# Kernel tuning notes

Hardware: AMD Instinct MI355X
Metric: run time of the kernel (lower is better)

The kernel has to match this reference:

```python
import jax, jax.numpy as jnp
import numpy as np

SOLVER_STEPS = 4  # fixed-step Euler steps per ODE solve (solver_step)


def setup_inputs() -> dict:
    key = jax.random.key(0)
    ks = jax.random.split(key, 10)
    B, T, D, H = 256, 1024, 128, 512
    sd = 1.0 / np.sqrt(H)
    n = lambda k, shape, scale: (jax.random.normal(k, shape, jnp.float32) * scale)
    return {
        "x": n(ks[0], (B, T, D), 1.0),
        "t": jax.random.uniform(ks[1], (B, T, 1), jnp.float32),
        # torch.nn.LSTMCell parameters (gate order: input, forget, cell, output)
        "W_ih": n(ks[2], (4 * H, D), sd),
        "W_hh": n(ks[3], (4 * H, H), sd),
        "b_ih": n(ks[4], (4 * H,), sd),
        "b_hh": n(ks[5], (4 * H,), sd),
        # DiffeqConcat drift MLP: (H+1) -> H -> H, Tanh activation
        "w1": n(ks[6], (H, H + 1), 1.0 / np.sqrt(H + 1)),
        "b1": n(ks[7], (H,), 0.01),
        "w2": n(ks[8], (H, H), sd),
        "b2": n(ks[9], (H,), 0.01),
    }


def _drift(y, s, w1, b1, w2, b2):
    # MLP(concat([s, y])): s is the (scalar) integration time in [0, 1]
    inp = jnp.concatenate([jnp.full_like(y[..., :1], s), y], axis=-1)
    return jnp.tanh(inp @ w1.T + b1) @ w2.T + b2


def _ode_evolve(h, t_i, w1, b1, w2, b2):
    # Integrate dy/ds = t_i * f(s, y) for s in [0, 1] with fixed-step Euler
    # (torchdiffeq time-rescaling trick used by ODEModel/DiffeqConcat).
    dt = 1.0 / SOLVER_STEPS
    y = h
    for k in range(SOLVER_STEPS):
        y = y + dt * t_i * _drift(y, k * dt, w1, b1, w2, b2)  # t_i: (B,1) broadcasts
    return y


def _lstm_cell(x_i, c, h, W_ih, W_hh, b_ih, b_hh):
    gates = x_i @ W_ih.T + b_ih + h @ W_hh.T + b_hh  # (B, 4H)
    i, f, g, o = jnp.split(gates, 4, axis=-1)
    c_new = jax.nn.sigmoid(f) * c + jax.nn.sigmoid(i) * jnp.tanh(g)
    h_new = jax.nn.sigmoid(o) * jnp.tanh(c_new)
    return c_new, h_new


def reference(x, t, W_ih, W_hh, b_ih, b_hh, w1, b1, w2, b2):
    B, T, D = x.shape
    H = W_hh.shape[1]

    def step(carry, inp):
        c, h = carry
        x_i, t_i = inp  # (B, D), (B, 1)
        h_pre = _ode_evolve(h, t_i, w1, b1, w2, b2)
        c, h = _lstm_cell(x_i, c, h, W_ih, W_hh, b_ih, b_hh)
        return (c, h), h_pre

    init = (jnp.zeros((B, H), x.dtype), jnp.zeros((B, H), x.dtype))
    xs = (jnp.swapaxes(x, 0, 1), jnp.swapaxes(t, 0, 1))  # time-major for scan
    _, hiddens = jax.lax.scan(step, init, xs)  # (T, B, H)
    return jnp.swapaxes(hiddens, 0, 1)  # (B, T, H)
```

## Files before the change

kernel.cpp:

```cpp
#include <hip/hip_runtime.h>
#include <stdint.h>

#define B_  256
#define T_  1024
#define D_  128
#define H_  512
#define G4_ 2048
#define BT_ (B_ * T_)

#define NG_ 16
#define NC_ 16

typedef unsigned short u16;
typedef __attribute__((ext_vector_type(8))) short    bf16x8;
typedef __attribute__((ext_vector_type(8))) u16      u16x8;
typedef __attribute__((ext_vector_type(4))) float    f32x4;
typedef __attribute__((ext_vector_type(4))) uint32_t u32x4;

static __device__ __forceinline__ u16 f2bf(float f) {
  uint32_t u = __builtin_bit_cast(uint32_t, f);
  u += 0x7FFFu + ((u >> 16) & 1u);
  return (u16)(u >> 16);
}

static __device__ __forceinline__ u16x8 pack8(float4 a, float4 b) {
  u16x8 p;
  p[0] = f2bf(a.x); p[1] = f2bf(a.y); p[2] = f2bf(a.z); p[3] = f2bf(a.w);
  p[4] = f2bf(b.x); p[5] = f2bf(b.y); p[6] = f2bf(b.z); p[7] = f2bf(b.w);
  return p;
}

static __device__ __forceinline__ float fast_sig(float x) {
  return 1.f / (1.f + __expf(-x));
}
static __device__ __forceinline__ float fast_tanh(float x) {
  return 1.f - 2.f / (__expf(2.f * x) + 1.f);
}

__global__ void prep_kernel(const float* __restrict__ Whh, const float* __restrict__ Wih,
                            const float* __restrict__ w1,  const float* __restrict__ w2,
                            const float* __restrict__ b_ih, const float* __restrict__ b_hh,
                            u16* __restrict__ Whh_bf, u16* __restrict__ Wih_bf,
                            u16* __restrict__ w1y_bf, u16* __restrict__ w2_bf,
                            float* __restrict__ w1s, float* __restrict__ bsum,
                            uint32_t* __restrict__ flags, float* __restrict__ Yd) {
  const int idx = blockIdx.x * blockDim.x + threadIdx.x;
  if (idx < G4_ * H_) Whh_bf[idx] = f2bf(Whh[idx]);
  if (idx < G4_ * D_) Wih_bf[idx] = f2bf(Wih[idx]);
  if (idx < H_ * H_) {
    const int n = idx >> 9, k = idx & 511;
    w1y_bf[idx] = f2bf(w1[n * 513 + 1 + k]);
    w2_bf[idx]  = f2bf(w2[idx]);
  }
  if (idx < H_)  w1s[idx]  = w1[idx * 513];
  if (idx < G4_) bsum[idx] = b_ih[idx] + b_hh[idx];
  if (idx < T_ * NG_ * 4) flags[idx] = 0;
  if (idx < B_ * H_) {
    const int b = idx >> 9, h = idx & 511;
    Yd[(size_t)b * T_ * H_ + h] = 0.f;
  }
}

__launch_bounds__(256)
__global__ void lstm_persist2(const float* __restrict__ x,
                              const u16* __restrict__ Whh_bf,
                              const u16* __restrict__ Wih_bf,
                              const float* __restrict__ bsum,
                              float* __restrict__ Yd,
                              u16* __restrict__ xchh,
                              uint32_t* __restrict__ flags) {
  __shared__ u16   As[16][648];
  __shared__ float Gs[4][16][34];

  const int tid  = threadIdx.x;
  const int lane = tid & 63;
  const int gw   = tid >> 6;
  const int w    = blockIdx.x;
  const int g    = (w & 7) * 2 + (w >> 7);
  const int c    = (w >> 3) & 15;
  const int br0  = g * 16;
  const int hc0  = c * 32;

  const int cl = lane & 15;
  const int ko = (lane >> 4) * 8;

  bf16x8 wf0[20], wf1[20];
  {
    const int j0 = gw * H_ + hc0 + cl;
#pragma unroll
    for (int kt = 0; kt < 16; ++kt) {
      wf0[kt] = *(const bf16x8*)(Whh_bf + (size_t)j0 * H_ + kt * 32 + ko);
      wf1[kt] = *(const bf16x8*)(Whh_bf + (size_t)(j0 + 16) * H_ + kt * 32 + ko);
    }
#pragma unroll
    for (int kt = 0; kt < 4; ++kt) {
      wf0[16 + kt] = *(const bf16x8*)(Wih_bf + (size_t)j0 * D_ + kt * 32 + ko);
      wf1[16 + kt] = *(const bf16x8*)(Wih_bf + (size_t)(j0 + 16) * D_ + kt * 32 + ko);
    }
  }

  const int er = tid >> 4;
  const int ec = (tid & 15) * 2;
  const int jb = hc0 + ec;
  float c0 = 0.f, c1 = 0.f;
  const float bi0 = bsum[jb],            bi1 = bsum[jb + 1];
  const float bf0 = bsum[H_ + jb],       bf1 = bsum[H_ + jb + 1];
  const float bg0 = bsum[2 * H_ + jb],   bg1 = bsum[2 * H_ + jb + 1];
  const float bo0 = bsum[3 * H_ + jb],   bo1 = bsum[3 * H_ + jb + 1];

  const int xr  = tid & 15,  xk  = tid >> 4;
  const int pr  = tid >> 4,  pcb = tid & 15;

  for (int s = 0; s < T_ - 1; ++s) {
    {
      const float4* x4 = (const float4*)(x + ((size_t)(br0 + xr) * T_ + s) * D_ + xk * 8);
      float4 a = x4[0], b = x4[1];
      *(u16x8*)&As[xr][512 + xk * 8] = pack8(a, b);
    }

    if (s == 0) {
      u16x8 z = {};
#pragma unroll
      for (int i = 0; i < 4; ++i) *(u16x8*)&As[pr][pcb * 32 + i * 8] = z;
    } else {
      const char* fp = (const char*)flags + ((size_t)s * NG_ + g) * 16;
      u32x4 f;
      do {
        asm volatile("global_load_dwordx4 %0, %1, off sc0 sc1\n\ts_waitcnt vmcnt(0)"
                     : "=&v"(f) : "v"(fp) : "memory");
      } while (f[0] != 0xA5A5A5A5u || f[1] != 0xA5A5A5A5u ||
               f[2] != 0xA5A5A5A5u || f[3] != 0xA5A5A5A5u);
      const char* hb = (const char*)xchh + (((size_t)(s & 1) * NG_ + g) << 14) + tid * 64;
      u32x4 h0, h1, h2, h3;
      asm volatile(
        "global_load_dwordx4 %0, %4, off sc0 sc1\n\t"
        "global_load_dwordx4 %1, %4, off offset:16 sc0 sc1\n\t"
        "global_load_dwordx4 %2, %4, off offset:32 sc0 sc1\n\t"
        "global_load_dwordx4 %3, %4, off offset:48 sc0 sc1\n\t"
        "s_waitcnt vmcnt(0)"
        : "=&v"(h0), "=&v"(h1), "=&v"(h2), "=&v"(h3)
        : "v"(hb) : "memory");
      *(u16x8*)&As[pr][pcb * 32]      = __builtin_bit_cast(u16x8, h0);
      *(u16x8*)&As[pr][pcb * 32 + 8]  = __builtin_bit_cast(u16x8, h1);
      *(u16x8*)&As[pr][pcb * 32 + 16] = __builtin_bit_cast(u16x8, h2);
      *(u16x8*)&As[pr][pcb * 32 + 24] = __builtin_bit_cast(u16x8, h3);
    }
    __syncthreads();

    f32x4 acc0 = {}, acc1 = {};
#pragma unroll
    for (int kt = 0; kt < 20; ++kt) {
      bf16x8 a = *(const bf16x8*)&As[cl][kt * 32 + ko];
      acc0 = __builtin_amdgcn_mfma_f32_16x16x32_bf16(a, wf0[kt], acc0, 0, 0, 0);
      acc1 = __builtin_amdgcn_mfma_f32_16x16x32_bf16(a, wf1[kt], acc1, 0, 0, 0);
    }

    {
      const int rr = (lane >> 4) * 4;
#pragma unroll
      for (int r = 0; r < 4; ++r) {
        Gs[gw][rr + r][cl]      = acc0[r];
        Gs[gw][rr + r][16 + cl] = acc1[r];
      }
    }
    __syncthreads();

    {
      const float2 gi = *(const float2*)&Gs[0][er][ec];
      const float2 gf = *(const float2*)&Gs[1][er][ec];
      const float2 gg = *(const float2*)&Gs[2][er][ec];
      const float2 go = *(const float2*)&Gs[3][er][ec];
      c0 = fast_sig(gf.x + bf0) * c0 + fast_sig(gi.x + bi0) * fast_tanh(gg.x + bg0);
      c1 = fast_sig(gf.y + bf1) * c1 + fast_sig(gi.y + bi1) * fast_tanh(gg.y + bg1);
      const float h0v = fast_sig(go.x + bo0) * fast_tanh(c0);
      const float h1v = fast_sig(go.y + bo1) * fast_tanh(c1);
      const uint32_t hw = ((uint32_t)f2bf(h1v) << 16) | f2bf(h0v);
      u16* dst16 = xchh + ((((size_t)((s + 1) & 1) * NG_ + g) * 16 + er) << 9) + jb;
      asm volatile("global_store_dword %0, %1, off sc0 sc1" :: "v"(dst16), "v"(hw) : "memory");
      float2 hv; hv.x = h0v; hv.y = h1v;
      *(float2*)(Yd + ((size_t)(br0 + er) * T_ + (s + 1)) * H_ + jb) = hv;
      asm volatile("s_waitcnt vmcnt(0)" ::: "memory");
    }
    __syncthreads();

    if (tid == 0) {
      const char* fb = (const char*)flags + ((size_t)(s + 1) * NG_ + g) * 16 + c;
      uint32_t pat = 0xA5u;
      asm volatile("global_store_byte %0, %1, off sc0 sc1" :: "v"(fb), "v"(pat) : "memory");
    }
  }
}

__launch_bounds__(512)
__global__ void ode_fused2(const float* __restrict__ tptr,
                           const u16* __restrict__ w1y,
                           const u16* __restrict__ w2v,
                           const float* __restrict__ b1,
                           const float* __restrict__ b2,
                           const float* __restrict__ w1s,
                           float* __restrict__ Yd) {
  __shared__ u16 At[64][520];

  const int tid  = threadIdx.x;
  const int lane = tid & 63;
  const int wv   = tid >> 6;
  const int n0w  = wv * 64;
  const size_t m0 = (size_t)blockIdx.x * 64;
  const int cl = lane & 15;
  const int rq = (lane >> 4) * 4;
  const int ko = (lane >> 4) * 8;

  float b1v[4], b2v[4], w1sv[4];
#pragma unroll
  for (int nf = 0; nf < 4; ++nf) {
    const int cg = n0w + nf * 16 + cl;
    b1v[nf] = b1[cg]; b2v[nf] = b2[cg]; w1sv[nf] = w1s[cg];
  }
  float tv[4][4];
#pragma unroll
  for (int mf = 0; mf < 4; ++mf)
#pragma unroll
    for (int r = 0; r < 4; ++r)
      tv[mf][r] = 0.25f * tptr[m0 + mf * 16 + rq + r];

  f32x4 Y[4][4];
#pragma unroll
  for (int mf = 0; mf < 4; ++mf)
#pragma unroll
    for (int nf = 0; nf < 4; ++nf)
#pragma unroll
      for (int r = 0; r < 4; ++r)
        Y[mf][nf][r] = Yd[(m0 + mf * 16 + rq + r) * 512 + n0w + nf * 16 + cl];

#define WRITE_AT(EXPR)                                                        \
  do {                                                                        \
    _Pragma("unroll") for (int mf = 0; mf < 4; ++mf)                          \
    _Pragma("unroll") for (int nf = 0; nf < 4; ++nf)                          \
    _Pragma("unroll") for (int r = 0; r < 4; ++r)                             \
      At[mf * 16 + rq + r][n0w + nf * 16 + cl] = f2bf(EXPR);                  \
  } while (0)

#define GEMM_DIRECT(WPTR, ACC)                                                \
  do {                                                                        \
    _Pragma("unroll 2") for (int cc = 0; cc < 16; ++cc) {                     \
      bf16x8 bfv[4], af[4];                                                   \
      _Pragma("unroll") for (int nf = 0; nf < 4; ++nf)                        \
        bfv[nf] = *(const bf16x8*)(WPTR + (size_t)(n0w + nf * 16 + cl) * 512  \
                                   + cc * 32 + ko);                           \
      _Pragma("unroll") for (int mf = 0; mf < 4; ++mf)                        \
        af[mf] = *(const bf16x8*)&At[mf * 16 + cl][cc * 32 + ko];             \
      _Pragma("unroll") for (int mf = 0; mf < 4; ++mf)                        \
      _Pragma("unroll") for (int nf = 0; nf < 4; ++nf)                        \
        ACC[mf][nf] = __builtin_amdgcn_mfma_f32_16x16x32_bf16(                \
            af[mf], bfv[nf], ACC[mf][nf], 0, 0, 0);                           \
    }                                                                         \
  } while (0)

  WRITE_AT(Y[mf][nf][r]);
  __syncthreads();

#pragma unroll
  for (int k = 0; k < 4; ++k) {
    const float sk = 0.25f * k;
    f32x4 acc[4][4] = {};
    GEMM_DIRECT(w1y, acc);
    __syncthreads();
    WRITE_AT(fast_tanh(acc[mf][nf][r] + b1v[nf] + sk * w1sv[nf]));
    __syncthreads();
    f32x4 acc2[4][4] = {};
    GEMM_DIRECT(w2v, acc2);
    __syncthreads();
#pragma unroll
    for (int mf = 0; mf < 4; ++mf)
#pragma unroll
      for (int nf = 0; nf < 4; ++nf)
#pragma unroll
        for (int r = 0; r < 4; ++r)
          Y[mf][nf][r] += tv[mf][r] * (acc2[mf][nf][r] + b2v[nf]);
    if (k < 3) {
      WRITE_AT(Y[mf][nf][r]);
      __syncthreads();
    }
  }
#undef GEMM_DIRECT
#undef WRITE_AT

#pragma unroll
  for (int mf = 0; mf < 4; ++mf)
#pragma unroll
    for (int nf = 0; nf < 4; ++nf)
#pragma unroll
      for (int r = 0; r < 4; ++r)
        Yd[(m0 + mf * 16 + rq + r) * 512 + n0w + nf * 16 + cl] = Y[mf][nf][r];
}

extern "C" void kernel_launch(void* const* d_in, const int* in_sizes, int n_in,
                              void* d_out, int out_size, void* d_ws, size_t ws_size,
                              hipStream_t stream) {
  const float* x    = (const float*)d_in[0];
  const float* t    = (const float*)d_in[1];
  const float* W_ih = (const float*)d_in[2];
  const float* W_hh = (const float*)d_in[3];
  const float* b_ih = (const float*)d_in[4];
  const float* b_hh = (const float*)d_in[5];
  const float* w1   = (const float*)d_in[6];
  const float* b1   = (const float*)d_in[7];
  const float* w2   = (const float*)d_in[8];
  const float* b2   = (const float*)d_in[9];
  float* Yd = (float*)d_out;

  char* ws = (char*)d_ws;
  size_t off = 0;
  auto alloc = [&](size_t bytes) {
    void* p = ws + off;
    off += (bytes + 255) & ~(size_t)255;
    return p;
  };
  u16*      Whh_bf = (u16*)alloc((size_t)G4_ * H_ * 2);
  u16*      Wih_bf = (u16*)alloc((size_t)G4_ * D_ * 2);
  u16*      w1y_bf = (u16*)alloc((size_t)H_ * H_ * 2);
  u16*      w2_bf  = (u16*)alloc((size_t)H_ * H_ * 2);
  float*    w1s    = (float*)alloc(H_ * 4);
  float*    bsum   = (float*)alloc(G4_ * 4);
  u16*      xchh   = (u16*)alloc((size_t)2 * NG_ * 16 * H_ * 2);
  uint32_t* flags  = (uint32_t*)alloc((size_t)T_ * NG_ * 16);

  prep_kernel<<<4096, 256, 0, stream>>>(W_hh, W_ih, w1, w2, b_ih, b_hh,
                                        Whh_bf, Wih_bf, w1y_bf, w2_bf, w1s, bsum, flags, Yd);

  lstm_persist2<<<dim3(NG_ * NC_), 256, 0, stream>>>(x, Whh_bf, Wih_bf, bsum, Yd, xchh, flags);

  ode_fused2<<<dim3(BT_ / 64), 512, 0, stream>>>(t, w1y_bf, w2_bf, b1, b2, w1s, Yd);
}
```

Before: 7.028 ms.

## Replace flag-based LSTM step handoff with tagged hidden-state words; pipeline ODE weight loads

The persistent LSTM kernel stops using a separate per-step flag array with a block barrier and a waitcnt before signalling. Each bf16 hidden value is now packed with a 16-bit step tag into a 32-bit word and written with a relaxed atomic 64-bit store. Consumers poll the hidden-state data directly until every tag matches the step, which removes one barrier and one serialized flag round trip per step at the cost of doubling the exchange buffer size. Separately, the ODE GEMM loop now double-buffers its weight fragment loads from global memory and the outer solver loop is no longer unrolled, which is meant to hide load latency while limiting register pressure.

Result: slower. 8.439 ms (+20.1%).

```diff
diff --git a/kernel.cpp b/kernel.cpp
--- a/kernel.cpp
+++ b/kernel.cpp
@@ -43,7 +43,7 @@
                             u16* __restrict__ Whh_bf, u16* __restrict__ Wih_bf,
                             u16* __restrict__ w1y_bf, u16* __restrict__ w2_bf,
                             float* __restrict__ w1s, float* __restrict__ bsum,
-                            uint32_t* __restrict__ flags, float* __restrict__ Yd) {
+                            uint32_t* __restrict__ xch32, float* __restrict__ Yd) {
   const int idx = blockIdx.x * blockDim.x + threadIdx.x;
   if (idx < G4_ * H_) Whh_bf[idx] = f2bf(Whh[idx]);
   if (idx < G4_ * D_) Wih_bf[idx] = f2bf(Wih[idx]);
@@ -54,21 +54,20 @@
   }
   if (idx < H_)  w1s[idx]  = w1[idx * 513];
   if (idx < G4_) bsum[idx] = b_ih[idx] + b_hh[idx];
-  if (idx < T_ * NG_ * 4) flags[idx] = 0;
+  if (idx < 2 * B_ * H_) xch32[idx] = 0;
   if (idx < B_ * H_) {
     const int b = idx >> 9, h = idx & 511;
     Yd[(size_t)b * T_ * H_ + h] = 0.f;
   }
 }
 
-__launch_bounds__(256)
-__global__ void lstm_persist2(const float* __restrict__ x,
+__launch_bounds__(256, 1)
+__global__ void lstm_persist3(const float* __restrict__ x,
                               const u16* __restrict__ Whh_bf,
                               const u16* __restrict__ Wih_bf,
                               const float* __restrict__ bsum,
                               float* __restrict__ Yd,
-                              u16* __restrict__ xchh,
-                              uint32_t* __restrict__ flags) {
+                              uint32_t* __restrict__ xch32) {
   __shared__ u16   As[16][648];
   __shared__ float Gs[4][16][34];
 
@@ -98,6 +97,7 @@
       wf1[16 + kt] = *(const bf16x8*)(Wih_bf + (size_t)(j0 + 16) * D_ + kt * 32 + ko);
     }
   }
+  asm volatile("" ::: "memory");
 
   const int er = tid >> 4;
   const int ec = (tid & 15) * 2;
@@ -108,8 +108,9 @@
   const float bg0 = bsum[2 * H_ + jb],   bg1 = bsum[2 * H_ + jb + 1];
   const float bo0 = bsum[3 * H_ + jb],   bo1 = bsum[3 * H_ + jb + 1];
 
-  const int xr  = tid & 15,  xk  = tid >> 4;
-  const int pr  = tid >> 4,  pcb = tid & 15;
+  const int xr   = tid & 15,  xk   = tid >> 4;
+  const int prow = tid >> 4;
+  const int pcb  = (tid & 15) * 32;
 
   for (int s = 0; s < T_ - 1; ++s) {
     {
@@ -121,29 +122,47 @@
     if (s == 0) {
       u16x8 z = {};
 #pragma unroll
-      for (int i = 0; i < 4; ++i) *(u16x8*)&As[pr][pcb * 32 + i * 8] = z;
+      for (int i = 0; i < 4; ++i) *(u16x8*)&As[prow][pcb + i * 8] = z;
     } else {
-      const char* fp = (const char*)flags + ((size_t)s * NG_ + g) * 16;
-      u32x4 f;
+      const char* base = (const char*)(xch32 + (((size_t)(s & 1) * NG_ + g) << 13)) + tid * 128;
+      const uint32_t want = (uint32_t)s;
+      u32x4 r0, r1, r2, r3, r4, r5, r6, r7;
+      bool ok;
       do {
-        asm volatile("global_load_dwordx4 %0, %1, off sc0 sc1\n\ts_waitcnt vmcnt(0)"
-                     : "=&v"(f) : "v"(fp) : "memory");
-      } while (f[0] != 0xA5A5A5A5u || f[1] != 0xA5A5A5A5u ||
-               f[2] != 0xA5A5A5A5u || f[3] != 0xA5A5A5A5u);
-      const char* hb = (const char*)xchh + (((size_t)(s & 1) * NG_ + g) << 14) + tid * 64;
-      u32x4 h0, h1, h2, h3;
-      asm volatile(
-        "global_load_dwordx4 %0, %4, off sc0 sc1\n\t"
-        "global_load_dwordx4 %1, %4, off offset:16 sc0 sc1\n\t"
-        "global_load_dwordx4 %2, %4, off offset:32 sc0 sc1\n\t"
-        "global_load_dwordx4 %3, %4, off offset:48 sc0 sc1\n\t"
-        "s_waitcnt vmcnt(0)"
-        : "=&v"(h0), "=&v"(h1), "=&v"(h2), "=&v"(h3)
-        : "v"(hb) : "memory");
-      *(u16x8*)&As[pr][pcb * 32]      = __builtin_bit_cast(u16x8, h0);
-      *(u16x8*)&As[pr][pcb * 32 + 8]  = __builtin_bit_cast(u16x8, h1);
-      *(u16x8*)&As[pr][pcb * 32 + 16] = __builtin_bit_cast(u16x8, h2);
-      *(u16x8*)&As[pr][pcb * 32 + 24] = __builtin_bit_cast(u16x8, h3);
+        asm volatile(
+          "global_load_dwordx4 %0, %8, off sc0 sc1\n\t"
+          "global_load_dwordx4 %1, %8, off offset:16 sc0 sc1\n\t"
+          "global_load_dwordx4 %2, %8, off offset:32 sc0 sc1\n\t"
+          "global_load_dwordx4 %3, %8, off offset:48 sc0 sc1\n\t"
+          "global_load_dwordx4 %4, %8, off offset:64 sc0 sc1\n\t"
+          "global_load_dwordx4 %5, %8, off offset:80 sc0 sc1\n\t"
+          "global_load_dwordx4 %6, %8, off offset:96 sc0 sc1\n\t"
+          "global_load_dwordx4 %7, %8, off offset:112 sc0 sc1\n\t"
+          "s_waitcnt vmcnt(0)"
+          : "=&v"(r0), "=&v"(r1), "=&v"(r2), "=&v"(r3),
+            "=&v"(r4), "=&v"(r5), "=&v"(r6), "=&v"(r7)
+          : "v"(base) : "memory");
+        ok = true;
+#pragma unroll
+        for (int i = 0; i < 4; ++i) {
+          ok = ok && ((r0[i] & 0xFFFFu) == want) && ((r1[i] & 0xFFFFu) == want)
+                  && ((r2[i] & 0xFFFFu) == want) && ((r3[i] & 0xFFFFu) == want)
+                  && ((r4[i] & 0xFFFFu) == want) && ((r5[i] & 0xFFFFu) == want)
+                  && ((r6[i] & 0xFFFFu) == want) && ((r7[i] & 0xFFFFu) == want);
+        }
+      } while (!ok);
+      u16x8 d0, d1, d2, d3;
+#pragma unroll
+      for (int i = 0; i < 4; ++i) {
+        d0[i] = (u16)(r0[i] >> 16); d0[4 + i] = (u16)(r1[i] >> 16);
+        d1[i] = (u16)(r2[i] >> 16); d1[4 + i] = (u16)(r3[i] >> 16);
+        d2[i] = (u16)(r4[i] >> 16); d2[4 + i] = (u16)(r5[i] >> 16);
+        d3[i] = (u16)(r6[i] >> 16); d3[4 + i] = (u16)(r7[i] >> 16);
+      }
+      *(u16x8*)&As[prow][pcb]      = d0;
+      *(u16x8*)&As[prow][pcb + 8]  = d1;
+      *(u16x8*)&As[prow][pcb + 16] = d2;
+      *(u16x8*)&As[prow][pcb + 24] = d3;
     }
     __syncthreads();
 
@@ -174,25 +193,20 @@
       c1 = fast_sig(gf.y + bf1) * c1 + fast_sig(gi.y + bi1) * fast_tanh(gg.y + bg1);
       const float h0v = fast_sig(go.x + bo0) * fast_tanh(c0);
       const float h1v = fast_sig(go.y + bo1) * fast_tanh(c1);
-      const uint32_t hw = ((uint32_t)f2bf(h1v) << 16) | f2bf(h0v);
-      u16* dst16 = xchh + ((((size_t)((s + 1) & 1) * NG_ + g) * 16 + er) << 9) + jb;
-      asm volatile("global_store_dword %0, %1, off sc0 sc1" :: "v"(dst16), "v"(hw) : "memory");
+      const uint32_t tag = (uint32_t)(s + 1);
+      const uint32_t lo  = ((uint32_t)f2bf(h0v) << 16) | tag;
+      const uint32_t hi  = ((uint32_t)f2bf(h1v) << 16) | tag;
+      __hip_atomic_store(
+          (uint64_t*)(xch32 + (((size_t)((s + 1) & 1) * NG_ + g) << 13) + (er << 9) + jb),
+          ((uint64_t)hi << 32) | lo, __ATOMIC_RELAXED, __HIP_MEMORY_SCOPE_AGENT);
       float2 hv; hv.x = h0v; hv.y = h1v;
       *(float2*)(Yd + ((size_t)(br0 + er) * T_ + (s + 1)) * H_ + jb) = hv;
-      asm volatile("s_waitcnt vmcnt(0)" ::: "memory");
-    }
-    __syncthreads();
-
-    if (tid == 0) {
-      const char* fb = (const char*)flags + ((size_t)(s + 1) * NG_ + g) * 16 + c;
-      uint32_t pat = 0xA5u;
-      asm volatile("global_store_byte %0, %1, off sc0 sc1" :: "v"(fb), "v"(pat) : "memory");
     }
   }
 }
 
 __launch_bounds__(512)
-__global__ void ode_fused2(const float* __restrict__ tptr,
+__global__ void ode_fused3(const float* __restrict__ tptr,
                            const u16* __restrict__ w1y,
                            const u16* __restrict__ w2v,
                            const float* __restrict__ b1,
@@ -240,35 +254,43 @@
       At[mf * 16 + rq + r][n0w + nf * 16 + cl] = f2bf(EXPR);                  \
   } while (0)
 
-#define GEMM_DIRECT(WPTR, ACC)                                                \
+#define GEMM_PIPE(WPTR, ACC)                                                  \
   do {                                                                        \
-    _Pragma("unroll 2") for (int cc = 0; cc < 16; ++cc) {                     \
-      bf16x8 bfv[4], af[4];                                                   \
-      _Pragma("unroll") for (int nf = 0; nf < 4; ++nf)                        \
-        bfv[nf] = *(const bf16x8*)(WPTR + (size_t)(n0w + nf * 16 + cl) * 512  \
-                                   + cc * 32 + ko);                           \
+    const u16* wbase = (WPTR) + (size_t)(n0w + cl) * 512 + ko;                \
+    bf16x8 bv[2][4];                                                          \
+    _Pragma("unroll") for (int nf = 0; nf < 4; ++nf) {                        \
+      bv[0][nf] = *(const bf16x8*)(wbase + nf * 16 * 512);                    \
+      bv[1][nf] = *(const bf16x8*)(wbase + nf * 16 * 512 + 32);               \
+    }                                                                         \
+    _Pragma("unroll") for (int cc = 0; cc < 16; ++cc) {                       \
+      bf16x8 af[4];                                                           \
       _Pragma("unroll") for (int mf = 0; mf < 4; ++mf)                        \
         af[mf] = *(const bf16x8*)&At[mf * 16 + cl][cc * 32 + ko];             \
       _Pragma("unroll") for (int mf = 0; mf < 4; ++mf)                        \
       _Pragma("unroll") for (int nf = 0; nf < 4; ++nf)                        \
         ACC[mf][nf] = __builtin_amdgcn_mfma_f32_16x16x32_bf16(                \
-            af[mf], bfv[nf], ACC[mf][nf], 0, 0, 0);                           \
+            af[mf], bv[cc & 1][nf], ACC[mf][nf], 0, 0, 0);                    \
+      if (cc < 14) {                                                          \
+        _Pragma("unroll") for (int nf = 0; nf < 4; ++nf)                      \
+          bv[cc & 1][nf] =                                                    \
+              *(const bf16x8*)(wbase + nf * 16 * 512 + (cc + 2) * 32);        \
+      }                                                                       \
     }                                                                         \
   } while (0)
 
   WRITE_AT(Y[mf][nf][r]);
   __syncthreads();
 
-#pragma unroll
+#pragma unroll 1
   for (int k = 0; k < 4; ++k) {
     const float sk = 0.25f * k;
     f32x4 acc[4][4] = {};
-    GEMM_DIRECT(w1y, acc);
+    GEMM_PIPE(w1y, acc);
     __syncthreads();
     WRITE_AT(fast_tanh(acc[mf][nf][r] + b1v[nf] + sk * w1sv[nf]));
     __syncthreads();
     f32x4 acc2[4][4] = {};
-    GEMM_DIRECT(w2v, acc2);
+    GEMM_PIPE(w2v, acc2);
     __syncthreads();
 #pragma unroll
     for (int mf = 0; mf < 4; ++mf)
@@ -282,7 +304,7 @@
       __syncthreads();
     }
   }
-#undef GEMM_DIRECT
+#undef GEMM_PIPE
 #undef WRITE_AT
 
 #pragma unroll
@@ -322,13 +344,12 @@
   u16*      w2_bf  = (u16*)alloc((size_t)H_ * H_ * 2);
   float*    w1s    = (float*)alloc(H_ * 4);
   float*    bsum   = (float*)alloc(G4_ * 4);
-  u16*      xchh   = (u16*)alloc((size_t)2 * NG_ * 16 * H_ * 2);
-  uint32_t* flags  = (uint32_t*)alloc((size_t)T_ * NG_ * 16);
+  uint32_t* xch32  = (uint32_t*)alloc((size_t)2 * B_ * H_ * 4);
 
   prep_kernel<<<4096, 256, 0, stream>>>(W_hh, W_ih, w1, w2, b_ih, b_hh,
-                                        Whh_bf, Wih_bf, w1y_bf, w2_bf, w1s, bsum, flags, Yd);
-
-  lstm_persist2<<<dim3(NG_ * NC_), 256, 0, stream>>>(x, Whh_bf, Wih_bf, bsum, Yd, xchh, flags);
-
-  ode_fused2<<<dim3(BT_ / 64), 512, 0, stream>>>(t, w1y_bf, w2_bf, b1, b2, w1s, Yd);
-}
+                                        Whh_bf, Wih_bf, w1y_bf, w2_bf, w1s, bsum, xch32, Yd);
+
+  lstm_persist3<<<dim3(NG_ * NC_), 256, 0, stream>>>(x, Whh_bf, Wih_bf, bsum, Yd, xch32);
+
+  ode_fused3<<<dim3(BT_ / 64), 512, 0, stream>>>(t, w1y_bf, w2_bf, b1, b2, w1s, Yd);
+}
```
